# Optimization experiments

Measured on AMD Instinct MI355X. Metric: run time of the kernel, lower is better.

## Reference

```python
import jax, jax.numpy as jnp
import numpy as np
from jax import lax

D_MODEL = 128
D_INNER = 256      # expand=2 * d_model
D_STATE = 4
D_CONV = 4
DT_RANK = 16       # ceil(d_inner / 16), mamba-ssm default for the inner Mamba (expand=1)
DW_K = 3
B, H, W = 4, 64, 64


def setup_inputs() -> dict:
    key = jax.random.key(0)
    ks = jax.random.split(key, 16)
    g = lambda k, shape, s=0.02: jax.random.normal(k, shape, jnp.float32) * s
    inp = {}
    inp["x"] = jax.random.normal(ks[0], (B, D_MODEL, H, W), jnp.float32)
    inp["norm1_g"] = jnp.ones((D_MODEL,), jnp.float32)
    inp["norm1_b"] = jnp.zeros((D_MODEL,), jnp.float32)
    inp["in_proj_w"] = g(ks[1], (D_INNER, D_MODEL))
    inp["dwconv_w"] = g(ks[2], (D_INNER, 1, DW_K, DW_K), 0.1)
    # 4 independent Mamba modules (lr, rl, tb, bt), params stacked on axis 0
    inp["m_in_w"] = g(ks[3], (4, 2 * D_INNER, D_INNER))
    inp["m_conv_w"] = g(ks[4], (4, D_INNER, 1, D_CONV), 0.1)
    inp["m_conv_b"] = g(ks[5], (4, D_INNER), 0.1)
    inp["m_xproj_w"] = g(ks[6], (4, DT_RANK + 2 * D_STATE, D_INNER))
    inp["m_dt_w"] = g(ks[7], (4, D_INNER, DT_RANK), 0.1)
    inp["m_dt_b"] = jax.random.uniform(ks[8], (4, D_INNER), jnp.float32, -4.0, -2.0)
    inp["m_A_log"] = jnp.log(jnp.broadcast_to(
        jnp.arange(1, D_STATE + 1, dtype=jnp.float32), (4, D_INNER, D_STATE)))
    inp["m_D"] = jnp.ones((4, D_INNER), jnp.float32)
    inp["m_out_w"] = g(ks[9], (4, D_INNER, D_INNER))
    inp["normss_g"] = jnp.ones((D_INNER,), jnp.float32)
    inp["normss_b"] = jnp.zeros((D_INNER,), jnp.float32)
    inp["out_proj_w"] = g(ks[10], (D_MODEL, D_INNER))
    inp["norm2_g"] = jnp.ones((D_MODEL,), jnp.float32)
    inp["norm2_b"] = jnp.zeros((D_MODEL,), jnp.float32)
    inp["ffn_w1"] = g(ks[11], (D_MODEL, D_MODEL))
    inp["ffn_w2"] = g(ks[12], (D_MODEL, D_MODEL))
    return inp


def layer_norm(x, g, b, eps=1e-5):
    m = x.mean(-1, keepdims=True)
    v = ((x - m) ** 2).mean(-1, keepdims=True)
    return (x - m) * lax.rsqrt(v + eps) * g + b


def silu(x):
    return x * jax.nn.sigmoid(x)


def causal_dwconv1d(x, w, b):
    # x: (B, L, D); w: (D, 1, K) depthwise; left-pad K-1 (mamba pads both sides then truncates to L)
    xt = x.transpose(0, 2, 1)  # (B, D, L)
    y = lax.conv_general_dilated(xt, w, (1,), [(w.shape[-1] - 1, 0)],
                                 dimension_numbers=('NCH', 'OIH', 'NCH'),
                                 feature_group_count=xt.shape[1])
    return (y + b[None, :, None]).transpose(0, 2, 1)


def mamba(x, in_w, conv_w, conv_b, xproj_w, dt_w, dt_b, A_log, Dp, out_w):
    # x: (B, L, D) with D = D_INNER; inner Mamba has expand=1 so d_inner == d_model here
    Bb, L, Dm = x.shape
    xz = x @ in_w.T                                  # (B, L, 2D)
    xm, z = jnp.split(xz, 2, axis=-1)
    xm = silu(causal_dwconv1d(xm, conv_w, conv_b))   # (B, L, D)
    x_dbl = xm @ xproj_w.T                           # (B, L, dt_rank + 2N)
    dt = x_dbl[..., :DT_RANK]
    Bm = x_dbl[..., DT_RANK:DT_RANK + D_STATE]       # (B, L, N)
    Cm = x_dbl[..., DT_RANK + D_STATE:]              # (B, L, N)
    dt = jax.nn.softplus(dt @ dt_w.T + dt_b)         # (B, L, D)
    A = -jnp.exp(A_log)                              # (D, N)
    dA = jnp.exp(dt[..., None] * A)                  # (B, L, D, N)
    dBx = dt[..., None] * Bm[:, :, None, :] * xm[..., None]

    def step(h, inp):
        dA_t, dBx_t, C_t = inp
        h = dA_t * h + dBx_t                         # (B, D, N)
        return h, jnp.einsum('bdn,bn->bd', h, C_t)

    h0 = jnp.zeros((Bb, Dm, D_STATE), x.dtype)
    _, ys = lax.scan(step, h0, (dA.transpose(1, 0, 2, 3),
                                dBx.transpose(1, 0, 2, 3),
                                Cm.transpose(1, 0, 2)))
    y = ys.transpose(1, 0, 2) + Dp * xm              # (B, L, D)
    y = y * silu(z)
    return y @ out_w.T


def ss2d(h, Hh, Ww, mp):
    # h: (B, L, D). 4 directions: lr, rl (flip), tb (transpose), bt (transpose+flip)
    Bb, L, Dm = h.shape
    x_tb = h.reshape(Bb, Hh, Ww, Dm).transpose(0, 2, 1, 3).reshape(Bb, L, Dm)
    xs = jnp.stack([h, jnp.flip(h, 1), x_tb, jnp.flip(x_tb, 1)], 0)  # (4, B, L, D)
    ys = jax.vmap(mamba)(xs, *mp)                                     # (4, B, L, D)
    untb = lambda y: y.reshape(Bb, Ww, Hh, Dm).transpose(0, 2, 1, 3).reshape(Bb, L, Dm)
    y_lr = ys[0]
    y_rl = jnp.flip(ys[1], 1)
    y_tb = untb(ys[2])
    y_bt = untb(jnp.flip(ys[3], 1))
    return (y_lr + y_rl + y_tb + y_bt) / 4.0


def reference(x, norm1_g, norm1_b, in_proj_w, dwconv_w,
              m_in_w, m_conv_w, m_conv_b, m_xproj_w, m_dt_w, m_dt_b,
              m_A_log, m_D, m_out_w,
              normss_g, normss_b, out_proj_w,
              norm2_g, norm2_b, ffn_w1, ffn_w2):
    Bb, C, Hh, Ww = x.shape
    L = Hh * Ww
    x_flat = x.transpose(0, 2, 3, 1).reshape(Bb, L, C)
    x1 = layer_norm(x_flat, norm1_g, norm1_b)
    h = x1 @ in_proj_w.T                             # (B, L, d_inner)
    h2d = h.reshape(Bb, Hh, Ww, D_INNER).transpose(0, 3, 1, 2)
    p = DW_K // 2
    h2d = lax.conv_general_dilated(h2d, dwconv_w, (1, 1), [(p, p), (p, p)],
                                   dimension_numbers=('NCHW', 'OIHW', 'NCHW'),
                                   feature_group_count=D_INNER)
    h = silu(h2d.transpose(0, 2, 3, 1).reshape(Bb, L, D_INNER))
    mp = (m_in_w, m_conv_w, m_conv_b, m_xproj_w, m_dt_w, m_dt_b, m_A_log, m_D, m_out_w)
    h = ss2d(h, Hh, Ww, mp)
    h = layer_norm(h, normss_g, normss_b)
    h = h @ out_proj_w.T
    x2 = x_flat + h
    h2 = jax.nn.gelu(layer_norm(x2, norm2_g, norm2_b) @ ffn_w1.T, approximate=False) @ ffn_w2.T
    y = x2 + h2
    return y.reshape(Bb, Hh, Ww, C).transpose(0, 3, 1, 2)
```

## Files before the change

kernel.cpp:

```cpp
#include <hip/hip_runtime.h>
#include <math.h>


#define B_N   4
#define CDM   128
#define HH    64
#define WW    64
#define LL    4096
#define DI    256
#define DS    4
#define DCV   4
#define DTR   16
#define CS    32
#define NC    (LL / CS)
#define BLT   16384

typedef float    f32x4  __attribute__((ext_vector_type(4)));
typedef __bf16   bf16x8 __attribute__((ext_vector_type(8)));

__device__ __forceinline__ float silu_f(float x) { return x / (1.f + __expf(-x)); }
__device__ __forceinline__ float softplus_f(float x) {
  return fmaxf(x, 0.f) + __logf(1.f + __expf(-fabsf(x)));
}
__device__ __forceinline__ float gelu_f(float x) {
  return 0.5f * x * (1.f + erff(x * 0.70710678118654752f));
}
__device__ __forceinline__ ushort f2bf(float x) {
  unsigned u = __builtin_bit_cast(unsigned, x);
  u += 0x7fffu + ((u >> 16) & 1u);
  return (ushort)(u >> 16);
}
__device__ __forceinline__ float bf2f(ushort u) {
  return __builtin_bit_cast(float, (unsigned)u << 16);
}

__device__ __forceinline__ int sigma_map(int dir, int t) {
  int tt = (dir & 1) ? (LL - 1 - t) : t;
  if (dir >= 2) tt = ((tt & 63) << 6) | (tt >> 6);
  return tt;
}

#define GLDS(gp, lp) __builtin_amdgcn_global_load_lds( \
    (const __attribute__((address_space(1))) void*)(gp), \
    (__attribute__((address_space(3))) void*)(lp), 16, 0, 0)

__global__ void __launch_bounds__(256) k_cvt(
    const float* __restrict__ s0, const float* __restrict__ s1,
    const float* __restrict__ s2, const float* __restrict__ s3,
    const float* __restrict__ s4, const float* __restrict__ s5,
    ushort* __restrict__ dst)
{
  int i = (blockIdx.x * 256 + threadIdx.x) * 4;
  const float* s; int base;
  if      (i < 32768)  { s = s0; base = 0; }
  else if (i < 557056) { s = s1; base = 32768; }
  else if (i < 819200) { s = s2; base = 557056; }
  else if (i < 851968) { s = s3; base = 819200; }
  else if (i < 868352) { s = s4; base = 851968; }
  else if (i < 884736) { s = s5; base = 868352; }
  else return;
  float4 v = *(const float4*)(s + (i - base));
  dst[i+0] = f2bf(v.x); dst[i+1] = f2bf(v.y); dst[i+2] = f2bf(v.z); dst[i+3] = f2bf(v.w);
}

__global__ void __launch_bounds__(256) k_dteff(
    const float* __restrict__ dtw, const float* __restrict__ xpw,
    ushort* __restrict__ w_dt, ushort* __restrict__ w_bc)
{
  int idx = blockIdx.x * 256 + threadIdx.x;
  if (idx >= 4 * 272 * 256) return;
  int dir = idx / 69632; int rem = idx - dir * 69632;
  int n = rem >> 8; int k = rem & 255;
  if (n < 256) {
    const float* dw = dtw + ((size_t)dir * DI + n) * DTR;
    const float* xp = xpw + (size_t)dir * 6144 + k;
    float acc = 0.f;
    #pragma unroll
    for (int j = 0; j < DTR; ++j) acc += dw[j] * xp[j * DI];
    w_dt[(size_t)dir * 65536 + (size_t)n * 256 + k] = f2bf(acc);
  } else {
    int n2 = n - 256;
    float v = (n2 < 8) ? xpw[(size_t)dir * 6144 + (size_t)(16 + n2) * 256 + k] : 0.f;
    w_bc[(size_t)dir * 4096 + (size_t)n2 * 256 + k] = f2bf(v);
  }
}

__global__ void __launch_bounds__(256) k_ln1(
    const float* __restrict__ x, const float* __restrict__ g,
    const float* __restrict__ be, float* __restrict__ xflat,
    ushort* __restrict__ x1b)
{
  int blk = blockIdx.x;
  int b = blk >> 6; int l0 = (blk & 63) << 6;
  __shared__ float T[64][129];
  __shared__ float mrow[64], rrow[64];
  int t = threadIdx.x;
  int wv = t >> 6, lane = t & 63;
  for (int c = wv; c < CDM; c += 4)
    T[lane][c] = x[((size_t)b * CDM + c) * LL + l0 + lane];
  __syncthreads();
  int row = t >> 2, seg = t & 3;
  float s = 0.f;
  #pragma unroll
  for (int j = 0; j < 32; ++j) s += T[row][seg * 32 + j];
  s += __shfl_xor(s, 1); s += __shfl_xor(s, 2);
  float mean = s * (1.f / CDM);
  float v2 = 0.f;
  #pragma unroll
  for (int j = 0; j < 32; ++j) { float d = T[row][seg * 32 + j] - mean; v2 += d * d; }
  v2 += __shfl_xor(v2, 1); v2 += __shfl_xor(v2, 2);
  if (seg == 0) { mrow[row] = mean; rrow[row] = rsqrtf(v2 * (1.f / CDM) + 1e-5f); }
  __syncthreads();
  int c = t & 127;
  float gc = g[c], bc = be[c];
  for (int r = (t >> 7); r < 64; r += 2) {
    float v = T[r][c];
    size_t o = ((size_t)(b << 12) + l0 + r) * CDM + c;
    xflat[o] = v;
    x1b[o] = f2bf((v - mrow[r]) * rrow[r] * gc + bc);
  }
}

__global__ void __launch_bounds__(256) k_lnw256(
    const ushort* __restrict__ in, const float* __restrict__ g,
    const float* __restrict__ be, ushort* __restrict__ out)
{
  int w = threadIdx.x >> 6, lane = threadIdx.x & 63;
  int row = (blockIdx.x << 2) + w;
  size_t off = (size_t)row * DI + (lane << 2);
  ushort4 v4 = *(const ushort4*)(in + off);
  float v0 = bf2f(v4.x), v1 = bf2f(v4.y), v2 = bf2f(v4.z), v3 = bf2f(v4.w);
  float s1 = v0 + v1 + v2 + v3;
  float s2 = v0 * v0 + v1 * v1 + v2 * v2 + v3 * v3;
  #pragma unroll
  for (int o = 1; o < 64; o <<= 1) { s1 += __shfl_xor(s1, o); s2 += __shfl_xor(s2, o); }
  float mean = s1 * (1.f / DI);
  float r = rsqrtf(s2 * (1.f / DI) - mean * mean + 1e-5f);
  int c = lane << 2;
  ushort4 o4;
  o4.x = f2bf((v0 - mean) * r * g[c + 0] + be[c + 0]);
  o4.y = f2bf((v1 - mean) * r * g[c + 1] + be[c + 1]);
  o4.z = f2bf((v2 - mean) * r * g[c + 2] + be[c + 2]);
  o4.w = f2bf((v3 - mean) * r * g[c + 3] + be[c + 3]);
  *(ushort4*)(out + off) = o4;
}

__global__ void __launch_bounds__(256) k_lnw128(
    const float* __restrict__ in, const float* __restrict__ g,
    const float* __restrict__ be, ushort* __restrict__ out)
{
  int w = threadIdx.x >> 6, lane = threadIdx.x & 63;
  int row = (blockIdx.x << 2) + w;
  size_t off = (size_t)row * CDM + (lane << 1);
  float2 v = *(const float2*)(in + off);
  float s1 = v.x + v.y;
  float s2 = v.x * v.x + v.y * v.y;
  #pragma unroll
  for (int o = 1; o < 64; o <<= 1) { s1 += __shfl_xor(s1, o); s2 += __shfl_xor(s2, o); }
  float mean = s1 * (1.f / CDM);
  float r = rsqrtf(s2 * (1.f / CDM) - mean * mean + 1e-5f);
  int c = lane << 1;
  ushort2 o2;
  o2.x = f2bf((v.x - mean) * r * g[c + 0] + be[c + 0]);
  o2.y = f2bf((v.y - mean) * r * g[c + 1] + be[c + 1]);
  *(ushort2*)(out + off) = o2;
}

template<int GATHER, int EPI, int BZ>
__global__ void __launch_bounds__(256) k_mgemm(
    const ushort* __restrict__ A, int lda,
    const ushort* __restrict__ Wt,
    float* __restrict__ Cf, ushort* __restrict__ Cb,
    int ldc, int K, const float* __restrict__ aux)
{
  if (BZ) {
    int z = blockIdx.z;
    A  += (size_t)z * BLT * DI;
    Wt += (size_t)z * DI * DI;
    if (Cb) Cb += (size_t)z * BLT * DI;
    if (aux) aux += (size_t)z * DI;
  }
  __shared__ ushort SH[16384];
  int tid = threadIdx.x;
  int m0 = blockIdx.x << 7, n0 = blockIdx.y << 7;
  int lane = tid & 63;
  int wm = ((tid >> 7) & 1) * 64;
  int wn = ((tid >> 6) & 1) * 64;
  int r15 = lane & 15, khi = lane >> 4;

  int srow = tid >> 3;
  int scol = (tid & 7) << 3;
  int arow[4], wrow[4];
  #pragma unroll
  for (int i = 0; i < 4; ++i) { arow[i] = m0 + i * 32 + srow; wrow[i] = n0 + i * 32 + srow; }

  f32x4 acc[4][4] = {};
  int wavebase = (tid & 192) * 8;

  for (int ks = 0; ks < K; ks += 64) {
    if (ks) __syncthreads();
    int dir = (GATHER == 2) ? (ks >> 8) : 0;
    int kin = (GATHER == 2) ? (ks & 255) : ks;
    #pragma unroll
    for (int i = 0; i < 4; ++i) {
      const ushort* gA = (GATHER == 2)
          ? A + (size_t)dir * (BLT * DI) + (size_t)arow[i] * DI + kin + scol
          : A + (size_t)arow[i] * lda + kin + scol;
      GLDS(gA, SH + i * 2048 + wavebase);
    }
    #pragma unroll
    for (int i = 0; i < 4; ++i) {
      const ushort* gW = (GATHER == 2)
          ? Wt + (size_t)dir * (DI * DI) + (size_t)wrow[i] * DI + kin + scol
          : Wt + (size_t)wrow[i] * K + kin + scol;
      GLDS(gW, SH + 8192 + i * 2048 + wavebase);
    }
    __syncthreads();
    #pragma unroll
    for (int kk = 0; kk < 2; ++kk) {
      bf16x8 af[4], wf[4];
      #pragma unroll
      for (int mi = 0; mi < 4; ++mi)
        af[mi] = *(const bf16x8*)&SH[(wm + mi * 16 + r15) * 64 + kk * 32 + khi * 8];
      #pragma unroll
      for (int ni = 0; ni < 4; ++ni)
        wf[ni] = *(const bf16x8*)&SH[8192 + (wn + ni * 16 + r15) * 64 + kk * 32 + khi * 8];
      #pragma unroll
      for (int mi = 0; mi < 4; ++mi)
        #pragma unroll
        for (int ni = 0; ni < 4; ++ni)
          acc[mi][ni] = __builtin_amdgcn_mfma_f32_16x16x32_bf16(
              af[mi], wf[ni], acc[mi][ni], 0, 0, 0);
    }
  }

  if (EPI == 3) {
    #pragma unroll
    for (int mi = 0; mi < 4; ++mi)
      #pragma unroll
      for (int j = 0; j < 4; ++j) {
        int row = m0 + wm + mi * 16 + khi * 4 + j;
        #pragma unroll
        for (int ni = 0; ni < 4; ++ni) {
          int col = n0 + wn + ni * 16 + r15;
          size_t off = (size_t)row * ldc + col;
          Cf[off] = aux[off] + acc[mi][ni][j];
        }
      }
    return;
  }
  __syncthreads();
  #pragma unroll
  for (int mi = 0; mi < 4; ++mi)
    #pragma unroll
    for (int j = 0; j < 4; ++j) {
      int rr = wm + mi * 16 + khi * 4 + j;
      int sw = (rr & 7) << 3;
      #pragma unroll
      for (int ni = 0; ni < 4; ++ni) {
        int cc = wn + ni * 16 + r15;
        float v = acc[mi][ni][j];
        ushort bvv;
        if      (EPI == 4)  bvv = f2bf(gelu_f(v));
        else if (EPI == 8)  bvv = f2bf(0.25f * v);
        else if (EPI == 10) bvv = f2bf(softplus_f(v + aux[n0 + cc]));
        else                bvv = f2bf(v);
        SH[rr * 128 + (cc ^ sw)] = bvv;
      }
    }
  __syncthreads();
  #pragma unroll
  for (int i = 0; i < 8; ++i) {
    int rr = i * 16 + (tid >> 4);
    int cc = (tid & 15) << 3;
    uint4 v = *(const uint4*)&SH[rr * 128 + (cc ^ ((rr & 7) << 3))];
    *(uint4*)&Cb[(size_t)(m0 + rr) * ldc + n0 + cc] = v;
  }
}

__global__ void __launch_bounds__(256) k_dwconv(
    const ushort* __restrict__ h, const float* __restrict__ wgt,
    ushort* __restrict__ out)
{
  int p = blockIdx.x;
  int b = p >> 12; int l = p & (LL - 1);
  int hy = l >> 6, wx = l & 63;
  int d = threadIdx.x;
  float acc = 0.f;
  #pragma unroll
  for (int di = -1; di <= 1; ++di) {
    int yy = hy + di; if (yy < 0 || yy >= HH) continue;
    #pragma unroll
    for (int dj = -1; dj <= 1; ++dj) {
      int xx = wx + dj; if (xx < 0 || xx >= WW) continue;
      acc += wgt[d * 9 + (di + 1) * 3 + (dj + 1)] *
             bf2f(h[(((size_t)b << 12) + (yy << 6) + xx) * DI + d]);
    }
  }
  out[(size_t)p * DI + d] = f2bf(silu_f(acc));
}

__global__ void __launch_bounds__(256) k_conv1d4(
    const ushort* __restrict__ xz_all, const float* __restrict__ cw,
    const float* __restrict__ cb, ushort* __restrict__ xmc4)
{
  int blk = blockIdx.x;
  int dir = blk >> 8; int b = (blk >> 6) & 3; int ch = blk & 63;
  int t0 = ch << 6;
  int d = threadIdx.x;
  const float* cwd = cw + (dir * DI + d) * DCV;
  float w0 = cwd[0], w1 = cwd[1], w2 = cwd[2], w3 = cwd[3];
  float bias = cb[dir * DI + d];
  size_t colb = (size_t)(dir << 9) + d;
  size_t rowb = (size_t)(b << 12);
  float xm3 = 0.f, xm2 = 0.f, xm1 = 0.f;
  if (t0 >= 3) {
    xm3 = bf2f(xz_all[(rowb + sigma_map(dir, t0 - 3)) * 2048 + colb]);
    xm2 = bf2f(xz_all[(rowb + sigma_map(dir, t0 - 2)) * 2048 + colb]);
    xm1 = bf2f(xz_all[(rowb + sigma_map(dir, t0 - 1)) * 2048 + colb]);
  }
  size_t obase = ((size_t)dir * BLT + (b << 12) + t0) * DI + d;
  #pragma unroll 4
  for (int i = 0; i < 64; ++i) {
    int l = sigma_map(dir, t0 + i);
    float x0 = bf2f(xz_all[(rowb + l) * 2048 + colb]);
    float acc = bias + w0 * xm3 + w1 * xm2 + w2 * xm1 + w3 * x0;
    xm3 = xm2; xm2 = xm1; xm1 = x0;
    xmc4[obase + (size_t)i * DI] = f2bf(silu_f(acc));
  }
}

__global__ void __launch_bounds__(256) k_bc(
    const ushort* __restrict__ xmc4, const ushort* __restrict__ w_bc,
    float* __restrict__ xbc4)
{
  __shared__ ushort As[128 * 64];
  __shared__ ushort Bs[16 * 64];
  int blk = blockIdx.x;
  int dir = blk >> 7; int m0 = (blk & 127) << 7;
  int tid = threadIdx.x;
  int lane = tid & 63; int wv = tid >> 6;
  int r15 = lane & 15, khi = lane >> 4;
  int srow = tid >> 3, scol = (tid & 7) << 3;
  size_t abase = (size_t)dir * BLT * DI;
  f32x4 acc[2] = {};
  for (int ks = 0; ks < 256; ks += 64) {
    if (ks) __syncthreads();
    #pragma unroll
    for (int i = 0; i < 4; ++i) {
      const ushort* g = xmc4 + abase + (size_t)(m0 + i * 32 + srow) * DI + ks + scol;
      GLDS(g, As + i * 2048 + tid * 8);
    }
    if (tid < 128) {
      const ushort* g = w_bc + (size_t)dir * 4096 + (size_t)(tid >> 3) * 256 + ks + scol;
      GLDS(g, Bs + tid * 8);
    }
    __syncthreads();
    #pragma unroll
    for (int kk = 0; kk < 2; ++kk) {
      bf16x8 af0 = *(const bf16x8*)&As[((wv << 5) + r15) * 64 + kk * 32 + khi * 8];
      bf16x8 af1 = *(const bf16x8*)&As[((wv << 5) + 16 + r15) * 64 + kk * 32 + khi * 8];
      bf16x8 wf  = *(const bf16x8*)&Bs[r15 * 64 + kk * 32 + khi * 8];
      acc[0] = __builtin_amdgcn_mfma_f32_16x16x32_bf16(af0, wf, acc[0], 0, 0, 0);
      acc[1] = __builtin_amdgcn_mfma_f32_16x16x32_bf16(af1, wf, acc[1], 0, 0, 0);
    }
  }
  if (r15 < 8) {
    #pragma unroll
    for (int mi = 0; mi < 2; ++mi)
      #pragma unroll
      for (int j = 0; j < 4; ++j) {
        int row = m0 + (wv << 5) + mi * 16 + khi * 4 + j;
        xbc4[((size_t)dir * BLT + row) * 8 + r15] = acc[mi][j];
      }
  }
}

__global__ void __launch_bounds__(256) k_scan_part(
    const ushort* __restrict__ dt4, const ushort* __restrict__ xmc4,
    const float* __restrict__ xbc4, const float* __restrict__ Alog4,
    float* __restrict__ P4, float* __restrict__ H4)
{
  int blk = blockIdx.x;
  int dir = blk >> 9; int b = (blk >> 7) & 3; int ch = blk & (NC - 1);
  int d = threadIdx.x;
  const float* Alog = Alog4 + (size_t)dir * DI * DS;
  float Av[DS], h[DS], P[DS];
  #pragma unroll
  for (int n = 0; n < DS; ++n) { Av[n] = -__expf(Alog[d * DS + n]); h[n] = 0.f; P[n] = 1.f; }
  size_t seg = (size_t)dir * BLT;
  size_t base = seg + (size_t)b * LL + (size_t)ch * CS;
  #pragma unroll 4
  for (int t = 0; t < CS; ++t) {
    size_t r = base + t;
    float dt = bf2f(dt4[r * DI + d]);
    float xm = bf2f(xmc4[r * DI + d]);
    float4 Bv = *(const float4*)(xbc4 + r * 8);
    float bx = dt * xm;
    float dA0 = __expf(dt * Av[0]), dA1 = __expf(dt * Av[1]);
    float dA2 = __expf(dt * Av[2]), dA3 = __expf(dt * Av[3]);
    h[0] = dA0 * h[0] + bx * Bv.x; P[0] *= dA0;
    h[1] = dA1 * h[1] + bx * Bv.y; P[1] *= dA1;
    h[2] = dA2 * h[2] + bx * Bv.z; P[2] *= dA2;
    h[3] = dA3 * h[3] + bx * Bv.w; P[3] *= dA3;
  }
  size_t o = ((size_t)blk * DI + d) * DS;
  #pragma unroll
  for (int n = 0; n < DS; ++n) { P4[o + n] = P[n]; H4[o + n] = h[n]; }
}

__global__ void __launch_bounds__(256) k_scan_carry(
    const float* __restrict__ P4, float* __restrict__ H4)
{
  int idx = blockIdx.x * 256 + threadIdx.x;
  int dir = idx >> 12; int r = idx & 4095;
  int b = r >> 10; int dn = r & 1023;
  size_t sbase = ((size_t)dir * 512 + (size_t)b * NC) * 1024 + dn;
  float carry = 0.f;
  #pragma unroll 8
  for (int ch = 0; ch < NC; ++ch) {
    size_t o = sbase + (size_t)ch * 1024;
    float Pv = P4[o], Hv = H4[o];
    H4[o] = carry;
    carry = Pv * carry + Hv;
  }
}

__global__ void __launch_bounds__(256) k_scan_fix(
    const ushort* __restrict__ dt4, const ushort* __restrict__ xmc4,
    const float* __restrict__ xbc4, const ushort* __restrict__ xz_all,
    const float* __restrict__ Alog4, const float* __restrict__ Dp4,
    const float* __restrict__ Cin, ushort* __restrict__ ybuf4)
{
  int blk = blockIdx.x;
  int dir = blk >> 9; int b = (blk >> 7) & 3; int ch = blk & (NC - 1);
  int d = threadIdx.x;
  const float* Alog = Alog4 + (size_t)dir * DI * DS;
  float Av[DS], h[DS];
  size_t ci = ((size_t)blk * DI + d) * DS;
  #pragma unroll
  for (int n = 0; n < DS; ++n) { Av[n] = -__expf(Alog[d * DS + n]); h[n] = Cin[ci + n]; }
  float Dv = Dp4[dir * DI + d];
  size_t seg = (size_t)dir * BLT;
  size_t base = seg + (size_t)b * LL + (size_t)ch * CS;
  #pragma unroll 4
  for (int t = 0; t < CS; ++t) {
    size_t r = base + t;
    float dt = bf2f(dt4[r * DI + d]);
    float xm = bf2f(xmc4[r * DI + d]);
    float4 Bv = *(const float4*)(xbc4 + r * 8);
    float4 Cv = *(const float4*)(xbc4 + r * 8 + 4);
    float bx = dt * xm;
    float dA0 = __expf(dt * Av[0]), dA1 = __expf(dt * Av[1]);
    float dA2 = __expf(dt * Av[2]), dA3 = __expf(dt * Av[3]);
    h[0] = dA0 * h[0] + bx * Bv.x;
    h[1] = dA1 * h[1] + bx * Bv.y;
    h[2] = dA2 * h[2] + bx * Bv.z;
    h[3] = dA3 * h[3] + bx * Bv.w;
    float y = h[0] * Cv.x + h[1] * Cv.y + h[2] * Cv.z + h[3] * Cv.w;
    int l = sigma_map(dir, (ch << 5) + t);
    float zv = bf2f(xz_all[(((size_t)(b << 12)) + l) * 2048 + (dir << 9) + 256 + d]);
    ybuf4[(seg + (size_t)(b << 12) + l) * DI + d] = f2bf((y + Dv * xm) * silu_f(zv));
  }
}

__global__ void __launch_bounds__(256) k_out_tr(
    const float* __restrict__ yfin, float* __restrict__ out)
{
  int b = blockIdx.x, c0 = blockIdx.y << 6, l0 = blockIdx.z << 6;
  __shared__ float T[64][65];
  int t = threadIdx.x;
  int q = t >> 6, lane = t & 63;
  for (int i = q; i < 64; i += 4)
    T[i][lane] = yfin[((size_t)(b << 12) + l0 + i) * CDM + c0 + lane];
  __syncthreads();
  for (int cc = q; cc < 64; cc += 4)
    out[(((size_t)b * CDM + c0 + cc) << 12) + l0 + lane] = T[lane][cc];
}

extern "C" void kernel_launch(void* const* d_in, const int* in_sizes, int n_in,
                              void* d_out, int out_size, void* d_ws, size_t ws_size,
                              hipStream_t stream) {
  const float* x          = (const float*)d_in[0];
  const float* norm1_g    = (const float*)d_in[1];
  const float* norm1_b    = (const float*)d_in[2];
  const float* in_proj_w  = (const float*)d_in[3];
  const float* dwconv_w   = (const float*)d_in[4];
  const float* m_in_w     = (const float*)d_in[5];
  const float* m_conv_w   = (const float*)d_in[6];
  const float* m_conv_b   = (const float*)d_in[7];
  const float* m_xproj_w  = (const float*)d_in[8];
  const float* m_dt_w     = (const float*)d_in[9];
  const float* m_dt_b     = (const float*)d_in[10];
  const float* m_A_log    = (const float*)d_in[11];
  const float* m_D        = (const float*)d_in[12];
  const float* m_out_w    = (const float*)d_in[13];
  const float* normss_g   = (const float*)d_in[14];
  const float* normss_b   = (const float*)d_in[15];
  const float* out_proj_w = (const float*)d_in[16];
  const float* norm2_g    = (const float*)d_in[17];
  const float* norm2_b    = (const float*)d_in[18];
  const float* ffn_w1     = (const float*)d_in[19];
  const float* ffn_w2     = (const float*)d_in[20];

  float* ws = (float*)d_ws;
  size_t o = 0;
  auto alloc = [&](size_t nf) { float* p = ws + o; o += nf; return p; };
  const size_t BL = BLT;
  float* xflat = alloc(BL * CDM);
  float* x2    = alloc(BL * CDM);
  float* yfin  = alloc(BL * CDM);
  float* xbc4  = alloc(BL * 8 * 4);
  float* P4    = alloc((size_t)4 * B_N * NC * DI * DS);
  float* H4    = alloc((size_t)4 * B_N * NC * DI * DS);
  auto ualloc = [&](size_t nu) { ushort* p = (ushort*)(ws + o); o += (nu + 1) / 2; return p; };
  ushort* x1b    = ualloc(BL * CDM);
  ushort* hinb   = ualloc(BL * DI);
  ushort* hcb    = ualloc(BL * DI);
  ushort* xz_all = ualloc(BL * 2048);
  ushort* xmc4   = ualloc(BL * DI * 4);
  ushort* dt4    = ualloc(BL * DI * 4);
  ushort* ybuf4  = ualloc(BL * DI * 4);
  ushort* ycombb = ualloc(BL * DI);
  ushort* hlnb   = ualloc(BL * DI);
  ushort* x3b    = ualloc(BL * CDM);
  ushort* f1b    = ualloc(BL * CDM);
  ushort* wb     = ualloc(884736);
  ushort* w_dt   = ualloc((size_t)4 * DI * DI);
  ushort* w_bc   = ualloc((size_t)4 * 16 * DI);
  ushort* w_inproj = wb + 0;
  ushort* w_min    = wb + 32768;
  ushort* w_mout   = wb + 557056;
  ushort* w_oproj  = wb + 819200;
  ushort* w_ffn1   = wb + 851968;
  ushort* w_ffn2   = wb + 868352;

  k_cvt<<<864, 256, 0, stream>>>(
      in_proj_w, m_in_w, m_out_w, out_proj_w, ffn_w1, ffn_w2, wb);
  k_dteff<<<1088, 256, 0, stream>>>(m_dt_w, m_xproj_w, w_dt, w_bc);
  k_ln1<<<B_N * 64, 256, 0, stream>>>(x, norm1_g, norm1_b, xflat, x1b);
  k_mgemm<0, 6, 0><<<dim3(128, 2), 256, 0, stream>>>(
      x1b, CDM, w_inproj, nullptr, hinb, DI, CDM, nullptr);
  k_dwconv<<<B_N * LL, DI, 0, stream>>>(hinb, dwconv_w, hcb);
  k_mgemm<0, 6, 0><<<dim3(128, 16), 256, 0, stream>>>(
      hcb, DI, w_min, nullptr, xz_all, 2048, DI, nullptr);
  k_conv1d4<<<1024, 256, 0, stream>>>(xz_all, m_conv_w, m_conv_b, xmc4);
  k_mgemm<0, 10, 1><<<dim3(128, 2, 4), 256, 0, stream>>>(
      xmc4, DI, w_dt, nullptr, dt4, DI, DI, m_dt_b);
  k_bc<<<512, 256, 0, stream>>>(xmc4, w_bc, xbc4);
  k_scan_part<<<4 * B_N * NC, 256, 0, stream>>>(dt4, xmc4, xbc4, m_A_log, P4, H4);
  k_scan_carry<<<64, 256, 0, stream>>>(P4, H4);
  k_scan_fix<<<4 * B_N * NC, 256, 0, stream>>>(
      dt4, xmc4, xbc4, xz_all, m_A_log, m_D, H4, ybuf4);
  k_mgemm<2, 8, 0><<<dim3(128, 2), 256, 0, stream>>>(
      ybuf4, DI, w_mout, nullptr, ycombb, DI, 1024, nullptr);
  k_lnw256<<<BLT / 4, 256, 0, stream>>>(ycombb, normss_g, normss_b, hlnb);
  k_mgemm<0, 3, 0><<<dim3(128, 1), 256, 0, stream>>>(
      hlnb, DI, w_oproj, x2, nullptr, CDM, DI, xflat);
  k_lnw128<<<BLT / 4, 256, 0, stream>>>(x2, norm2_g, norm2_b, x3b);
  k_mgemm<0, 4, 0><<<dim3(128, 1), 256, 0, stream>>>(
      x3b, CDM, w_ffn1, nullptr, f1b, CDM, CDM, nullptr);
  k_mgemm<0, 3, 0><<<dim3(128, 1), 256, 0, stream>>>(
      f1b, CDM, w_ffn2, yfin, nullptr, CDM, CDM, x2);
  k_out_tr<<<dim3(B_N, 2, 64), 256, 0, stream>>>(yfin, (float*)d_out);
}
```

Baseline: 285.2 us.

## Fuse out-proj with residual+LN2, FFN with transpose output, merge prep kernels

Merges the weight-conversion and dt-weight precompute kernels into one launch. Fuses the out_proj GEMM with the residual add and second layer norm, using 64-row tiles so each block holds full rows. Fuses both FFN GEMMs, GELU, the residual and the NCHW transpose into one kernel that keeps the intermediate activation in LDS. This removes several launches and round trips of intermediates through global memory, but the 64-row tiles mean only 256 blocks with a smaller MFMA tile per wave.

```diff
diff --git a/kernel.cpp b/kernel.cpp
--- a/kernel.cpp
+++ b/kernel.cpp
@@ -44,44 +44,44 @@
     (const __attribute__((address_space(1))) void*)(gp), \
     (__attribute__((address_space(3))) void*)(lp), 16, 0, 0)
 
-__global__ void __launch_bounds__(256) k_cvt(
+__global__ void __launch_bounds__(256) k_prep(
     const float* __restrict__ s0, const float* __restrict__ s1,
     const float* __restrict__ s2, const float* __restrict__ s3,
     const float* __restrict__ s4, const float* __restrict__ s5,
-    ushort* __restrict__ dst)
-{
-  int i = (blockIdx.x * 256 + threadIdx.x) * 4;
-  const float* s; int base;
-  if      (i < 32768)  { s = s0; base = 0; }
-  else if (i < 557056) { s = s1; base = 32768; }
-  else if (i < 819200) { s = s2; base = 557056; }
-  else if (i < 851968) { s = s3; base = 819200; }
-  else if (i < 868352) { s = s4; base = 851968; }
-  else if (i < 884736) { s = s5; base = 868352; }
-  else return;
-  float4 v = *(const float4*)(s + (i - base));
-  dst[i+0] = f2bf(v.x); dst[i+1] = f2bf(v.y); dst[i+2] = f2bf(v.z); dst[i+3] = f2bf(v.w);
-}
-
-__global__ void __launch_bounds__(256) k_dteff(
+    ushort* __restrict__ dst,
     const float* __restrict__ dtw, const float* __restrict__ xpw,
     ushort* __restrict__ w_dt, ushort* __restrict__ w_bc)
 {
-  int idx = blockIdx.x * 256 + threadIdx.x;
-  if (idx >= 4 * 272 * 256) return;
-  int dir = idx / 69632; int rem = idx - dir * 69632;
-  int n = rem >> 8; int k = rem & 255;
-  if (n < 256) {
-    const float* dw = dtw + ((size_t)dir * DI + n) * DTR;
-    const float* xp = xpw + (size_t)dir * 6144 + k;
-    float acc = 0.f;
-    #pragma unroll
-    for (int j = 0; j < DTR; ++j) acc += dw[j] * xp[j * DI];
-    w_dt[(size_t)dir * 65536 + (size_t)n * 256 + k] = f2bf(acc);
+  int blk = blockIdx.x;
+  if (blk < 864) {
+    int i = (blk * 256 + threadIdx.x) * 4;
+    const float* s; int base;
+    if      (i < 32768)  { s = s0; base = 0; }
+    else if (i < 557056) { s = s1; base = 32768; }
+    else if (i < 819200) { s = s2; base = 557056; }
+    else if (i < 851968) { s = s3; base = 819200; }
+    else if (i < 868352) { s = s4; base = 851968; }
+    else if (i < 884736) { s = s5; base = 868352; }
+    else return;
+    float4 v = *(const float4*)(s + (i - base));
+    dst[i+0] = f2bf(v.x); dst[i+1] = f2bf(v.y); dst[i+2] = f2bf(v.z); dst[i+3] = f2bf(v.w);
   } else {
-    int n2 = n - 256;
-    float v = (n2 < 8) ? xpw[(size_t)dir * 6144 + (size_t)(16 + n2) * 256 + k] : 0.f;
-    w_bc[(size_t)dir * 4096 + (size_t)n2 * 256 + k] = f2bf(v);
+    int idx = (blk - 864) * 256 + threadIdx.x;
+    if (idx >= 4 * 272 * 256) return;
+    int dir = idx / 69632; int rem = idx - dir * 69632;
+    int n = rem >> 8; int k = rem & 255;
+    if (n < 256) {
+      const float* dw = dtw + ((size_t)dir * DI + n) * DTR;
+      const float* xp = xpw + (size_t)dir * 6144 + k;
+      float acc = 0.f;
+      #pragma unroll
+      for (int j = 0; j < DTR; ++j) acc += dw[j] * xp[j * DI];
+      w_dt[(size_t)dir * 65536 + (size_t)n * 256 + k] = f2bf(acc);
+    } else {
+      int n2 = n - 256;
+      float v = (n2 < 8) ? xpw[(size_t)dir * 6144 + (size_t)(16 + n2) * 256 + k] : 0.f;
+      w_bc[(size_t)dir * 4096 + (size_t)n2 * 256 + k] = f2bf(v);
+    }
   }
 }
 
@@ -145,27 +145,6 @@
   *(ushort4*)(out + off) = o4;
 }
 
-__global__ void __launch_bounds__(256) k_lnw128(
-    const float* __restrict__ in, const float* __restrict__ g,
-    const float* __restrict__ be, ushort* __restrict__ out)
-{
-  int w = threadIdx.x >> 6, lane = threadIdx.x & 63;
-  int row = (blockIdx.x << 2) + w;
-  size_t off = (size_t)row * CDM + (lane << 1);
-  float2 v = *(const float2*)(in + off);
-  float s1 = v.x + v.y;
-  float s2 = v.x * v.x + v.y * v.y;
-  #pragma unroll
-  for (int o = 1; o < 64; o <<= 1) { s1 += __shfl_xor(s1, o); s2 += __shfl_xor(s2, o); }
-  float mean = s1 * (1.f / CDM);
-  float r = rsqrtf(s2 * (1.f / CDM) - mean * mean + 1e-5f);
-  int c = lane << 1;
-  ushort2 o2;
-  o2.x = f2bf((v.x - mean) * r * g[c + 0] + be[c + 0]);
-  o2.y = f2bf((v.y - mean) * r * g[c + 1] + be[c + 1]);
-  *(ushort2*)(out + off) = o2;
-}
-
 template<int GATHER, int EPI, int BZ>
 __global__ void __launch_bounds__(256) k_mgemm(
     const ushort* __restrict__ A, int lda,
@@ -234,21 +213,6 @@
     }
   }
 
-  if (EPI == 3) {
-    #pragma unroll
-    for (int mi = 0; mi < 4; ++mi)
-      #pragma unroll
-      for (int j = 0; j < 4; ++j) {
-        int row = m0 + wm + mi * 16 + khi * 4 + j;
-        #pragma unroll
-        for (int ni = 0; ni < 4; ++ni) {
-          int col = n0 + wn + ni * 16 + r15;
-          size_t off = (size_t)row * ldc + col;
-          Cf[off] = aux[off] + acc[mi][ni][j];
-        }
-      }
-    return;
-  }
   __syncthreads();
   #pragma unroll
   for (int mi = 0; mi < 4; ++mi)
@@ -261,8 +225,7 @@
         int cc = wn + ni * 16 + r15;
         float v = acc[mi][ni][j];
         ushort bvv;
-        if      (EPI == 4)  bvv = f2bf(gelu_f(v));
-        else if (EPI == 8)  bvv = f2bf(0.25f * v);
+        if      (EPI == 8)  bvv = f2bf(0.25f * v);
         else if (EPI == 10) bvv = f2bf(softplus_f(v + aux[n0 + cc]));
         else                bvv = f2bf(v);
         SH[rr * 128 + (cc ^ sw)] = bvv;
@@ -276,6 +239,198 @@
     uint4 v = *(const uint4*)&SH[rr * 128 + (cc ^ ((rr & 7) << 3))];
     *(uint4*)&Cb[(size_t)(m0 + rr) * ldc + n0 + cc] = v;
   }
+}
+
+__global__ void __launch_bounds__(256) k_oplna(
+    const ushort* __restrict__ A,
+    const ushort* __restrict__ Wt,
+    const float* __restrict__ xflat,
+    const float* __restrict__ g, const float* __restrict__ be,
+    float* __restrict__ x2, ushort* __restrict__ x3b)
+{
+  __shared__ ushort As[64 * 64];
+  __shared__ ushort Ws[128 * 64];
+  __shared__ float redA[64][2], redB[64][2];
+  int tid = threadIdx.x;
+  int m0 = blockIdx.x << 6;
+  int lane = tid & 63;
+  int wm = ((tid >> 7) & 1) * 32;
+  int wn = ((tid >> 6) & 1) * 64;
+  int r15 = lane & 15, khi = lane >> 4;
+  int srow = tid >> 3, scol = (tid & 7) << 3;
+
+  f32x4 acc[2][4] = {};
+  for (int ks = 0; ks < 256; ks += 64) {
+    if (ks) __syncthreads();
+    #pragma unroll
+    for (int i = 0; i < 2; ++i) {
+      const ushort* gA = A + (size_t)(m0 + i * 32 + srow) * DI + ks + scol;
+      GLDS(gA, As + i * 2048 + tid * 8);
+    }
+    #pragma unroll
+    for (int i = 0; i < 4; ++i) {
+      const ushort* gW = Wt + (size_t)(i * 32 + srow) * DI + ks + scol;
+      GLDS(gW, Ws + i * 2048 + tid * 8);
+    }
+    __syncthreads();
+    #pragma unroll
+    for (int kk = 0; kk < 2; ++kk) {
+      bf16x8 af[2], wf[4];
+      #pragma unroll
+      for (int mi = 0; mi < 2; ++mi)
+        af[mi] = *(const bf16x8*)&As[(wm + mi * 16 + r15) * 64 + kk * 32 + khi * 8];
+      #pragma unroll
+      for (int ni = 0; ni < 4; ++ni)
+        wf[ni] = *(const bf16x8*)&Ws[(wn + ni * 16 + r15) * 64 + kk * 32 + khi * 8];
+      #pragma unroll
+      for (int mi = 0; mi < 2; ++mi)
+        #pragma unroll
+        for (int ni = 0; ni < 4; ++ni)
+          acc[mi][ni] = __builtin_amdgcn_mfma_f32_16x16x32_bf16(
+              af[mi], wf[ni], acc[mi][ni], 0, 0, 0);
+    }
+  }
+  float vbuf[2][4][4];
+  #pragma unroll
+  for (int mi = 0; mi < 2; ++mi)
+    #pragma unroll
+    for (int j = 0; j < 4; ++j) {
+      int rr = wm + mi * 16 + khi * 4 + j;
+      float s1 = 0.f, s2 = 0.f;
+      #pragma unroll
+      for (int ni = 0; ni < 4; ++ni) {
+        int cc = wn + ni * 16 + r15;
+        float v = acc[mi][ni][j] + xflat[(size_t)(m0 + rr) * CDM + cc];
+        vbuf[mi][ni][j] = v;
+        s1 += v; s2 += v * v;
+      }
+      #pragma unroll
+      for (int o = 1; o < 16; o <<= 1) { s1 += __shfl_xor(s1, o); s2 += __shfl_xor(s2, o); }
+      if (r15 == 0) { redA[rr][wn >> 6] = s1; redB[rr][wn >> 6] = s2; }
+    }
+  __syncthreads();
+  #pragma unroll
+  for (int mi = 0; mi < 2; ++mi)
+    #pragma unroll
+    for (int j = 0; j < 4; ++j) {
+      int rr = wm + mi * 16 + khi * 4 + j;
+      float mean = (redA[rr][0] + redA[rr][1]) * (1.f / CDM);
+      float var  = (redB[rr][0] + redB[rr][1]) * (1.f / CDM) - mean * mean;
+      float rstd = rsqrtf(var + 1e-5f);
+      #pragma unroll
+      for (int ni = 0; ni < 4; ++ni) {
+        int cc = wn + ni * 16 + r15;
+        size_t off = (size_t)(m0 + rr) * CDM + cc;
+        float v = vbuf[mi][ni][j];
+        x2[off] = v;
+        x3b[off] = f2bf((v - mean) * rstd * g[cc] + be[cc]);
+      }
+    }
+}
+
+__global__ void __launch_bounds__(256) k_ffn(
+    const ushort* __restrict__ x3b, const ushort* __restrict__ w1,
+    const ushort* __restrict__ w2, const float* __restrict__ x2,
+    float* __restrict__ out)
+{
+  __shared__ ushort SH[20480];
+  ushort* stageA = SH;
+  ushort* stageW = SH + 4096;
+  ushort* f1     = SH + 12288;
+  float*  T      = (float*)SH;
+  int tid = threadIdx.x;
+  int m0 = blockIdx.x << 6;
+  int b = m0 >> 12, l0 = m0 & (LL - 1);
+  int lane = tid & 63;
+  int wm = ((tid >> 7) & 1) * 32;
+  int wn = ((tid >> 6) & 1) * 64;
+  int r15 = lane & 15, khi = lane >> 4;
+  int srow = tid >> 3, scol = (tid & 7) << 3;
+
+  f32x4 acc[2][4] = {};
+  for (int ks = 0; ks < 128; ks += 64) {
+    if (ks) __syncthreads();
+    #pragma unroll
+    for (int i = 0; i < 2; ++i)
+      GLDS(x3b + (size_t)(m0 + i * 32 + srow) * CDM + ks + scol, stageA + i * 2048 + tid * 8);
+    #pragma unroll
+    for (int i = 0; i < 4; ++i)
+      GLDS(w1 + (size_t)(i * 32 + srow) * CDM + ks + scol, stageW + i * 2048 + tid * 8);
+    __syncthreads();
+    #pragma unroll
+    for (int kk = 0; kk < 2; ++kk) {
+      bf16x8 af[2], wf[4];
+      #pragma unroll
+      for (int mi = 0; mi < 2; ++mi)
+        af[mi] = *(const bf16x8*)&stageA[(wm + mi * 16 + r15) * 64 + kk * 32 + khi * 8];
+      #pragma unroll
+      for (int ni = 0; ni < 4; ++ni)
+        wf[ni] = *(const bf16x8*)&stageW[(wn + ni * 16 + r15) * 64 + kk * 32 + khi * 8];
+      #pragma unroll
+      for (int mi = 0; mi < 2; ++mi)
+        #pragma unroll
+        for (int ni = 0; ni < 4; ++ni)
+          acc[mi][ni] = __builtin_amdgcn_mfma_f32_16x16x32_bf16(
+              af[mi], wf[ni], acc[mi][ni], 0, 0, 0);
+    }
+  }
+  __syncthreads();
+  #pragma unroll
+  for (int mi = 0; mi < 2; ++mi)
+    #pragma unroll
+    for (int j = 0; j < 4; ++j) {
+      int rr = wm + mi * 16 + khi * 4 + j;
+      int sw = (rr & 7) << 3;
+      #pragma unroll
+      for (int ni = 0; ni < 4; ++ni) {
+        int cc = wn + ni * 16 + r15;
+        f1[rr * 128 + (cc ^ sw)] = f2bf(gelu_f(acc[mi][ni][j]));
+      }
+    }
+  __syncthreads();
+  f32x4 acc2[2][4] = {};
+  for (int ks = 0; ks < 128; ks += 64) {
+    __syncthreads();
+    #pragma unroll
+    for (int i = 0; i < 4; ++i)
+      GLDS(w2 + (size_t)(i * 32 + srow) * CDM + ks + scol, stageW + i * 2048 + tid * 8);
+    __syncthreads();
+    #pragma unroll
+    for (int kk = 0; kk < 2; ++kk) {
+      bf16x8 af[2], wf[4];
+      #pragma unroll
+      for (int mi = 0; mi < 2; ++mi) {
+        int row = wm + mi * 16 + r15;
+        int kx = (ks + kk * 32 + khi * 8) ^ ((row & 7) << 3);
+        af[mi] = *(const bf16x8*)&f1[row * 128 + kx];
+      }
+      #pragma unroll
+      for (int ni = 0; ni < 4; ++ni)
+        wf[ni] = *(const bf16x8*)&stageW[(wn + ni * 16 + r15) * 64 + kk * 32 + khi * 8];
+      #pragma unroll
+      for (int mi = 0; mi < 2; ++mi)
+        #pragma unroll
+        for (int ni = 0; ni < 4; ++ni)
+          acc2[mi][ni] = __builtin_amdgcn_mfma_f32_16x16x32_bf16(
+              af[mi], wf[ni], acc2[mi][ni], 0, 0, 0);
+    }
+  }
+  __syncthreads();
+  #pragma unroll
+  for (int mi = 0; mi < 2; ++mi)
+    #pragma unroll
+    for (int j = 0; j < 4; ++j) {
+      int rr = wm + mi * 16 + khi * 4 + j;
+      #pragma unroll
+      for (int ni = 0; ni < 4; ++ni) {
+        int cc = wn + ni * 16 + r15;
+        T[rr * 129 + cc] = x2[(size_t)(m0 + rr) * CDM + cc] + acc2[mi][ni][j];
+      }
+    }
+  __syncthreads();
+  int q = tid >> 6;
+  for (int cc = q; cc < CDM; cc += 4)
+    out[(((size_t)b * CDM + cc) << 12) + l0 + lane] = T[lane * 129 + cc];
 }
 
 __global__ void __launch_bounds__(256) k_dwconv(
@@ -462,20 +617,6 @@
     float zv = bf2f(xz_all[(((size_t)(b << 12)) + l) * 2048 + (dir << 9) + 256 + d]);
     ybuf4[(seg + (size_t)(b << 12) + l) * DI + d] = f2bf((y + Dv * xm) * silu_f(zv));
   }
-}
-
-__global__ void __launch_bounds__(256) k_out_tr(
-    const float* __restrict__ yfin, float* __restrict__ out)
-{
-  int b = blockIdx.x, c0 = blockIdx.y << 6, l0 = blockIdx.z << 6;
-  __shared__ float T[64][65];
-  int t = threadIdx.x;
-  int q = t >> 6, lane = t & 63;
-  for (int i = q; i < 64; i += 4)
-    T[i][lane] = yfin[((size_t)(b << 12) + l0 + i) * CDM + c0 + lane];
-  __syncthreads();
-  for (int cc = q; cc < 64; cc += 4)
-    out[(((size_t)b * CDM + c0 + cc) << 12) + l0 + lane] = T[lane][cc];
 }
 
 extern "C" void kernel_launch(void* const* d_in, const int* in_sizes, int n_in,
@@ -509,7 +650,6 @@
   const size_t BL = BLT;
   float* xflat = alloc(BL * CDM);
   float* x2    = alloc(BL * CDM);
-  float* yfin  = alloc(BL * CDM);
   float* xbc4  = alloc(BL * 8 * 4);
   float* P4    = alloc((size_t)4 * B_N * NC * DI * DS);
   float* H4    = alloc((size_t)4 * B_N * NC * DI * DS);
@@ -524,7 +664,6 @@
   ushort* ycombb = ualloc(BL * DI);
   ushort* hlnb   = ualloc(BL * DI);
   ushort* x3b    = ualloc(BL * CDM);
-  ushort* f1b    = ualloc(BL * CDM);
   ushort* wb     = ualloc(884736);
   ushort* w_dt   = ualloc((size_t)4 * DI * DI);
   ushort* w_bc   = ualloc((size_t)4 * 16 * DI);
@@ -535,9 +674,9 @@
   ushort* w_ffn1   = wb + 851968;
   ushort* w_ffn2   = wb + 868352;
 
-  k_cvt<<<864, 256, 0, stream>>>(
-      in_proj_w, m_in_w, m_out_w, out_proj_w, ffn_w1, ffn_w2, wb);
-  k_dteff<<<1088, 256, 0, stream>>>(m_dt_w, m_xproj_w, w_dt, w_bc);
+  k_prep<<<1952, 256, 0, stream>>>(
+      in_proj_w, m_in_w, m_out_w, out_proj_w, ffn_w1, ffn_w2, wb,
+      m_dt_w, m_xproj_w, w_dt, w_bc);
   k_ln1<<<B_N * 64, 256, 0, stream>>>(x, norm1_g, norm1_b, xflat, x1b);
   k_mgemm<0, 6, 0><<<dim3(128, 2), 256, 0, stream>>>(
       x1b, CDM, w_inproj, nullptr, hinb, DI, CDM, nullptr);
@@ -555,12 +694,7 @@
   k_mgemm<2, 8, 0><<<dim3(128, 2), 256, 0, stream>>>(
       ybuf4, DI, w_mout, nullptr, ycombb, DI, 1024, nullptr);
   k_lnw256<<<BLT / 4, 256, 0, stream>>>(ycombb, normss_g, normss_b, hlnb);
-  k_mgemm<0, 3, 0><<<dim3(128, 1), 256, 0, stream>>>(
-      hlnb, DI, w_oproj, x2, nullptr, CDM, DI, xflat);
-  k_lnw128<<<BLT / 4, 256, 0, stream>>>(x2, norm2_g, norm2_b, x3b);
-  k_mgemm<0, 4, 0><<<dim3(128, 1), 256, 0, stream>>>(
-      x3b, CDM, w_ffn1, nullptr, f1b, CDM, CDM, nullptr);
-  k_mgemm<0, 3, 0><<<dim3(128, 1), 256, 0, stream>>>(
-      f1b, CDM, w_ffn2, yfin, nullptr, CDM, CDM, x2);
-  k_out_tr<<<dim3(B_N, 2, 64), 256, 0, stream>>>(yfin, (float*)d_out);
-}
+  k_oplna<<<256, 256, 0, stream>>>(
+      hlnb, w_oproj, xflat, norm2_g, norm2_b, x2, x3b);
+  k_ffn<<<256, 256, 0, stream>>>(x3b, w_ffn1, w_ffn2, x2, (float*)d_out);
+}
```

Result: faster. 249.4 us (-12.6%).
